# Performance work log

Measured on AMD Instinct MI355X. Metric: run time of the kernel, lower is better.

Reference implementation:

```python
import jax, jax.numpy as jnp
import numpy as np

N = 100000          # nodes
E = 3200000         # edges (avg degree 32)
IN = 256            # in_channels
H = 256             # hidden_channels == out_channels (PureConv identity lin)
STR = 60            # str_input
NUM_LOCAL = 8
NUM_LAYERS = 3


def setup_inputs() -> dict:
    key = jax.random.key(0)
    ks = jax.random.split(key, 8)
    x = jax.random.normal(ks[0], (N, IN), jnp.float32)
    pos_emb = jax.random.normal(ks[1], (N, STR), jnp.float32)
    lap_pe = jax.random.normal(ks[2], (N, STR - 1), jnp.float32)
    row = jax.random.randint(ks[3], (E,), 0, N, dtype=jnp.int32)
    col = jax.random.randint(ks[4], (E,), 0, N, dtype=jnp.int32)
    # learned params
    W_pos = jax.random.normal(ks[5], (2 * STR - 1, NUM_LOCAL), jnp.float32) * 0.1
    b_pos = jnp.zeros((NUM_LOCAL,), jnp.float32)
    W_xemb = jax.random.normal(ks[6], (IN + NUM_LOCAL, H), jnp.float32) * 0.05
    b_xemb = jnp.zeros((H,), jnp.float32)
    jkparams = jax.random.normal(ks[7], (NUM_LAYERS,), jnp.float32)
    return {
        "x": x, "pos_emb": pos_emb, "lap_pe": lap_pe,
        "W_pos": W_pos, "b_pos": b_pos, "W_xemb": W_xemb, "b_xemb": b_xemb,
        "jkparams": jkparams, "row": row, "col": col,
    }


def reference(x, pos_emb, lap_pe, W_pos, b_pos, W_xemb, b_xemb, jkparams, row, col):
    # pos_embedding: Linear(2*str_input-1 -> num_local) on cat([pos_emb, lap_pe])
    pe = jnp.concatenate([pos_emb, lap_pe], axis=-1) @ W_pos + b_pos      # [N, NUM_LOCAL]
    # xemb: Linear(in_channels + num_local -> hidden) (dropouts are identity, p=0)
    h = jnp.concatenate([x, pe], axis=-1) @ W_xemb + b_xemb               # [N, H]

    # GCN-style degree norm: norm = rsqrt(1 + rowsum(A))
    deg = jax.ops.segment_sum(jnp.ones((E,), h.dtype), row, num_segments=N)
    norm = jax.lax.rsqrt(1.0 + deg)[:, None]                              # [N, 1]

    jkx = []
    for _ in range(NUM_LAYERS):
        h = norm * h
        # spmm_add: (A @ h)[i] = sum_{edges (i<-j)} h[j]
        agg = jax.ops.segment_sum(h[col], row, num_segments=N)            # [N, H]
        h = norm * (agg + h)
        jkx.append(h)

    # jk weighted sum over layers
    out = jnp.sum(jnp.stack(jkx, axis=0) * jkparams[:, None, None], axis=0)
    return out
```

## Files before the change

kernel.cpp:

```cpp
#include <hip/hip_runtime.h>

constexpr int IN   = 256;
constexpr int H    = 256;
constexpr int STR  = 60;
constexpr int NLOC = 8;
constexpr int CHC  = 128;
constexpr int KP   = 288;
constexpr int CAP  = 96;

typedef float    f32x4 __attribute__((ext_vector_type(4)));
typedef unsigned u32x2 __attribute__((ext_vector_type(2)));
typedef short    bf16x8 __attribute__((ext_vector_type(8)));

__device__ __forceinline__ float bflo(unsigned u) { return __uint_as_float(u << 16); }
__device__ __forceinline__ float bfhi(unsigned u) { return __uint_as_float(u & 0xFFFF0000u); }
__device__ __forceinline__ unsigned short f2bf(float f) {
  unsigned u = __float_as_uint(f);
  u += 0x7FFF + ((u >> 16) & 1);
  return (unsigned short)(u >> 16);
}

__global__ void k_pe(const float* __restrict__ pos_emb, const float* __restrict__ lap_pe,
                     const float* __restrict__ W, const float* __restrict__ b,
                     float* __restrict__ pe, int n) {
  int i = blockIdx.x*blockDim.x + threadIdx.x;
  if (i >= n) return;
  float acc[NLOC];
  #pragma unroll
  for (int j = 0; j < NLOC; ++j) acc[j] = b[j];
  const float* pr = pos_emb + (size_t)i*STR;
  for (int k = 0; k < STR; ++k) {
    float v = pr[k];
    #pragma unroll
    for (int j = 0; j < NLOC; ++j) acc[j] += v*W[k*NLOC + j];
  }
  const float* lr = lap_pe + (size_t)i*(STR-1);
  for (int k = 0; k < STR-1; ++k) {
    float v = lr[k];
    #pragma unroll
    for (int j = 0; j < NLOC; ++j) acc[j] += v*W[(STR+k)*NLOC + j];
  }
  float* po = pe + (size_t)i*NLOC;
  #pragma unroll
  for (int j = 0; j < NLOC; ++j) po[j] = acc[j];
}

__global__ void k_wtb(const float* __restrict__ W, unsigned short* __restrict__ Wtb) {
  int col = blockIdx.x;
  for (int k = threadIdx.x; k < KP; k += blockDim.x) {
    float v = (k < IN + NLOC) ? W[(size_t)k*H + col] : 0.f;
    Wtb[(size_t)col*KP + k] = f2bf(v);
  }
}

__global__ void k_scatter(const int* __restrict__ row, const int* __restrict__ col,
                          int* __restrict__ cnt, int* __restrict__ colbuf, int E) {
  int i = blockIdx.x*blockDim.x + threadIdx.x;
  int stride = gridDim.x*blockDim.x;
  for (; i < E; i += stride) {
    int r = row[i];
    int p = atomicAdd(&cnt[r], 1);
    if (p < CAP) colbuf[(size_t)r*CAP + p] = col[i];
  }
}

__global__ void k_norm(const int* __restrict__ cnt, float* __restrict__ norm,
                       float* __restrict__ rnorm, int n) {
  int i = blockIdx.x*blockDim.x + threadIdx.x;
  if (i >= n) return;
  int d = cnt[i]; if (d > CAP) d = CAP;
  float s = 1.0f + (float)d;
  norm[i]  = rsqrtf(s);
  rnorm[i] = sqrtf(s);
}

__global__ __launch_bounds__(256) void k_xemb(
    const float* __restrict__ x, const float* __restrict__ pe,
    const unsigned short* __restrict__ Wtb, const float* __restrict__ bvec,
    const float* __restrict__ norm, unsigned short* __restrict__ st, int n) {
  int t = threadIdx.x;
  int wv = t >> 6, l = t & 63;
  int lr = l & 15, kb = l >> 4;
  int i0 = blockIdx.x*64 + wv*16;
  int arow = i0 + lr;
  int ar = (arow < n) ? arow : n - 1;

  f32x4 acc[16];
  #pragma unroll
  for (int cb = 0; cb < 16; ++cb) acc[cb] = (f32x4){0.f,0.f,0.f,0.f};

  const unsigned short* wb = Wtb + (size_t)lr*KP + kb*8;

  #pragma unroll
  for (int ks = 0; ks < 9; ++ks) {
    int k0 = ks*32;
    float a8[8];
    if (ks < 8) {
      const float* ap = x + (size_t)ar*IN + k0 + kb*8;
      float4 v0 = *(const float4*)ap;
      float4 v1 = *(const float4*)(ap + 4);
      a8[0]=v0.x; a8[1]=v0.y; a8[2]=v0.z; a8[3]=v0.w;
      a8[4]=v1.x; a8[5]=v1.y; a8[6]=v1.z; a8[7]=v1.w;
    } else if (kb == 0) {
      const float* ap = pe + (size_t)ar*NLOC;
      float4 v0 = *(const float4*)ap;
      float4 v1 = *(const float4*)(ap + 4);
      a8[0]=v0.x; a8[1]=v0.y; a8[2]=v0.z; a8[3]=v0.w;
      a8[4]=v1.x; a8[5]=v1.y; a8[6]=v1.z; a8[7]=v1.w;
    } else {
      #pragma unroll
      for (int j = 0; j < 8; ++j) a8[j] = 0.f;
    }
    bf16x8 af;
    #pragma unroll
    for (int j = 0; j < 8; ++j) af[j] = (short)f2bf(a8[j]);
    #pragma unroll
    for (int cb = 0; cb < 16; ++cb) {
      bf16x8 bf = *(const bf16x8*)(wb + (size_t)cb*16*KP + k0);
      acc[cb] = __builtin_amdgcn_mfma_f32_16x16x32_bf16(af, bf, acc[cb], 0, 0, 0);
    }
  }

  int r0 = i0 + kb*4;
  float nrm[4];
  #pragma unroll
  for (int j = 0; j < 4; ++j) {
    int rr = r0 + j;
    nrm[j] = (rr < n) ? norm[rr] : 0.f;
  }
  size_t slabsz = (size_t)n * CHC;
  #pragma unroll
  for (int cb = 0; cb < 16; ++cb) {
    int col = cb*16 + lr;
    float bias = bvec[col];
    unsigned short* sp = st + (size_t)(col >> 7)*slabsz + (col & 127);
    #pragma unroll
    for (int j = 0; j < 4; ++j) {
      int rr = r0 + j;
      if (rr < n)
        sp[(size_t)rr*CHC] = f2bf(nrm[j]*(acc[cb][j] + bias));
    }
  }
}

__global__ __launch_bounds__(256) void k_layer(
    const unsigned short* __restrict__ st, const int* __restrict__ cnt,
    const int* __restrict__ colbuf, const float* __restrict__ norm,
    unsigned short* __restrict__ st_next, int n, int nrb) {
  int w = blockIdx.x;
  int xcd = w & 7;
  int c = xcd >> 2;
  int rb = (w >> 3)*4 + (xcd & 3);
  if (rb >= nrb) return;
  int t = threadIdx.x;
  int wave = t >> 6, lane = t & 63, half = lane >> 5, li = lane & 31;
  int r = rb*8 + wave*2 + half;
  if (r >= n) return;
  size_t slab = (size_t)c * ((size_t)n * 32);
  const uint2* gb = (const uint2*)st + slab + li;
  int deg = cnt[r]; if (deg > CAP) deg = CAP;
  int start = r*CAP, end = start + deg;
  float4 acc = make_float4(0.f,0.f,0.f,0.f);
  int j = start;
  for (; j + 4 <= end; j += 4) {
    int c0 = colbuf[j],   c1 = colbuf[j+1];
    int c2 = colbuf[j+2], c3 = colbuf[j+3];
    uint2 v0 = gb[(size_t)c0*32];
    uint2 v1 = gb[(size_t)c1*32];
    uint2 v2 = gb[(size_t)c2*32];
    uint2 v3 = gb[(size_t)c3*32];
    acc.x += (bflo(v0.x)+bflo(v1.x)) + (bflo(v2.x)+bflo(v3.x));
    acc.y += (bfhi(v0.x)+bfhi(v1.x)) + (bfhi(v2.x)+bfhi(v3.x));
    acc.z += (bflo(v0.y)+bflo(v1.y)) + (bflo(v2.y)+bflo(v3.y));
    acc.w += (bfhi(v0.y)+bfhi(v1.y)) + (bfhi(v2.y)+bfhi(v3.y));
  }
  for (; j < end; ++j) {
    int c0 = colbuf[j];
    uint2 v0 = gb[(size_t)c0*32];
    acc.x += bflo(v0.x); acc.y += bfhi(v0.x);
    acc.z += bflo(v0.y); acc.w += bfhi(v0.y);
  }
  uint2 sv = gb[(size_t)r*32];
  acc.x += bflo(sv.x); acc.y += bfhi(sv.x);
  acc.z += bflo(sv.y); acc.w += bfhi(sv.y);
  float nr = norm[r];
  float n2 = nr*nr;
  unsigned short s0 = f2bf(n2*acc.x);
  unsigned short s1 = f2bf(n2*acc.y);
  unsigned short s2 = f2bf(n2*acc.z);
  unsigned short s3 = f2bf(n2*acc.w);
  u32x2 pk;
  pk.x = (unsigned)s0 | ((unsigned)s1 << 16);
  pk.y = (unsigned)s2 | ((unsigned)s3 << 16);
  __builtin_nontemporal_store(pk, (u32x2*)st_next + slab + (size_t)r*32 + li);
}

__global__ void k_jk(const unsigned short* __restrict__ s0,
                     const unsigned short* __restrict__ s1,
                     const unsigned short* __restrict__ s2,
                     const float* __restrict__ rnorm,
                     const float* __restrict__ jkp,
                     float* __restrict__ out, int n) {
  float j0 = jkp[0], j1 = jkp[1], j2 = jkp[2];
  size_t total = (size_t)n * 64;
  size_t idx = (size_t)blockIdx.x*blockDim.x + threadIdx.x;
  size_t stride = (size_t)gridDim.x*blockDim.x;
  for (; idx < total; idx += stride) {
    int r = (int)(idx >> 6);
    int g = (int)(idx & 63);
    int slab = g >> 5, cg = g & 31;
    size_t off = (size_t)slab*((size_t)n*32) + (size_t)r*32 + cg;
    uint2 a = ((const uint2*)s0)[off];
    uint2 b = ((const uint2*)s1)[off];
    uint2 c = ((const uint2*)s2)[off];
    float rn = rnorm[r];
    f32x4 o;
    o.x = rn*(j0*bflo(a.x) + j1*bflo(b.x) + j2*bflo(c.x));
    o.y = rn*(j0*bfhi(a.x) + j1*bfhi(b.x) + j2*bfhi(c.x));
    o.z = rn*(j0*bflo(a.y) + j1*bflo(b.y) + j2*bflo(c.y));
    o.w = rn*(j0*bfhi(a.y) + j1*bfhi(b.y) + j2*bfhi(c.y));
    *(f32x4*)(out + (size_t)r*H + slab*CHC + cg*4) = o;
  }
}

extern "C" void kernel_launch(void* const* d_in, const int* in_sizes, int n_in,
                              void* d_out, int out_size, void* d_ws, size_t ws_size,
                              hipStream_t stream) {
  const float* x       = (const float*)d_in[0];
  const float* pos_emb = (const float*)d_in[1];
  const float* lap_pe  = (const float*)d_in[2];
  const float* W_pos   = (const float*)d_in[3];
  const float* b_pos   = (const float*)d_in[4];
  const float* W_xemb  = (const float*)d_in[5];
  const float* b_xemb  = (const float*)d_in[6];
  const float* jkp     = (const float*)d_in[7];
  const int*   row     = (const int*)d_in[8];
  const int*   col     = (const int*)d_in[9];
  int N = in_sizes[0] / IN;
  int E = in_sizes[8];
  float* out = (float*)d_out;

  char* p = (char*)d_ws;
  auto alloc = [&](size_t bytes) {
    char* r = p; p += (bytes + 255) & ~(size_t)255; return r;
  };
  unsigned short* bfA = (unsigned short*)alloc((size_t)N*H*2);
  unsigned short* st0 = (unsigned short*)alloc((size_t)N*H*2);
  unsigned short* st2 = (unsigned short*)alloc((size_t)N*H*2);
  int*   colbuf = (int*)  alloc((size_t)N*CAP*4);
  float* pe     = (float*)alloc((size_t)N*NLOC*4);
  int*   cnt    = (int*)  alloc((size_t)N*4);
  float* norm   = (float*)alloc((size_t)N*4);
  float* rnorm  = (float*)alloc((size_t)N*4);
  unsigned short* Wtb = (unsigned short*)alloc((size_t)H*KP*2);

  hipMemsetAsync(cnt, 0, (size_t)N*4, stream);

  k_pe<<<(N+255)/256, 256, 0, stream>>>(pos_emb, lap_pe, W_pos, b_pos, pe, N);
  k_wtb<<<H, 128, 0, stream>>>(W_xemb, Wtb);
  k_scatter<<<2048, 256, 0, stream>>>(row, col, cnt, colbuf, E);
  k_norm<<<(N+255)/256, 256, 0, stream>>>(cnt, norm, rnorm, N);

  k_xemb<<<(N+63)/64, 256, 0, stream>>>(x, pe, Wtb, b_xemb, norm, bfA, N);

  int nrb = (N + 7)/8;
  int lgrid = 8 * ((nrb + 3)/4);
  k_layer<<<lgrid, 256, 0, stream>>>(bfA, cnt, colbuf, norm, st0, N, nrb);
  k_layer<<<lgrid, 256, 0, stream>>>(st0, cnt, colbuf, norm, bfA, N, nrb);
  k_layer<<<lgrid, 256, 0, stream>>>(bfA, cnt, colbuf, norm, st2, N, nrb);

  k_jk<<<2048, 256, 0, stream>>>(st0, bfA, st2, rnorm, jkp, out, N);
}
```

Measured before the change: 1.027 ms.

## Bucket edges before CSR fill and fuse JK sum into last layer

Edge-list construction becomes a two-pass bucketed scheme. Edges are first binned by row block of 256 into per-bucket buffers, then one workgroup per bucket fills the per-row column lists using LDS atomics and computes the degree norms in the same pass. This replaces the scattered global atomics and the separate norm kernel. The jumping-knowledge weighted sum is also fused into the third layer kernel, so the last layer's bf16 output is never written and re-read. The costs are an extra bin buffer with a fixed per-bucket capacity, which could overflow on skewed degree distributions, and a branch in the layer kernel.

```diff
diff --git a/kernel.cpp b/kernel.cpp
--- a/kernel.cpp
+++ b/kernel.cpp
@@ -7,6 +7,8 @@
 constexpr int CHC  = 128;
 constexpr int KP   = 288;
 constexpr int CAP  = 96;
+constexpr int RB   = 256;
+constexpr int BCAP = 10240;
 
 typedef float    f32x4 __attribute__((ext_vector_type(4)));
 typedef unsigned u32x2 __attribute__((ext_vector_type(2)));
@@ -53,25 +55,45 @@
   }
 }
 
-__global__ void k_scatter(const int* __restrict__ row, const int* __restrict__ col,
-                          int* __restrict__ cnt, int* __restrict__ colbuf, int E) {
+__global__ void k_bin(const int* __restrict__ row, const int* __restrict__ col,
+                      int* __restrict__ bcnt, uint2* __restrict__ binbuf, int E) {
   int i = blockIdx.x*blockDim.x + threadIdx.x;
   int stride = gridDim.x*blockDim.x;
   for (; i < E; i += stride) {
-    int r = row[i];
-    int p = atomicAdd(&cnt[r], 1);
-    if (p < CAP) colbuf[(size_t)r*CAP + p] = col[i];
-  }
-}
-
-__global__ void k_norm(const int* __restrict__ cnt, float* __restrict__ norm,
-                       float* __restrict__ rnorm, int n) {
-  int i = blockIdx.x*blockDim.x + threadIdx.x;
-  if (i >= n) return;
-  int d = cnt[i]; if (d > CAP) d = CAP;
-  float s = 1.0f + (float)d;
-  norm[i]  = rsqrtf(s);
-  rnorm[i] = sqrtf(s);
+    int r = row[i], c = col[i];
+    int b = r >> 8;
+    int p = atomicAdd(&bcnt[b], 1);
+    if (p < BCAP) binbuf[(size_t)b*BCAP + p] = make_uint2((unsigned)r, (unsigned)c);
+  }
+}
+
+__global__ __launch_bounds__(256) void k_fill(
+    const int* __restrict__ bcnt, const uint2* __restrict__ binbuf,
+    int* __restrict__ colbuf, int* __restrict__ cnt,
+    float* __restrict__ norm, float* __restrict__ rnorm, int n) {
+  __shared__ int lc[RB];
+  int b = blockIdx.x;
+  int t = threadIdx.x;
+  lc[t] = 0;
+  __syncthreads();
+  int base = b*RB;
+  int bc = bcnt[b]; if (bc > BCAP) bc = BCAP;
+  const uint2* bb = binbuf + (size_t)b*BCAP;
+  for (int i = t; i < bc; i += 256) {
+    uint2 e = bb[i];
+    int r = (int)e.x;
+    int p = atomicAdd(&lc[r - base], 1);
+    if (p < CAP) colbuf[(size_t)r*CAP + p] = (int)e.y;
+  }
+  __syncthreads();
+  int r = base + t;
+  if (r < n) {
+    int d = lc[t]; if (d > CAP) d = CAP;
+    cnt[r] = d;
+    float s = 1.0f + (float)d;
+    norm[r]  = rsqrtf(s);
+    rnorm[r] = sqrtf(s);
+  }
 }
 
 __global__ __launch_bounds__(256) void k_xemb(
@@ -146,7 +168,10 @@
 __global__ __launch_bounds__(256) void k_layer(
     const unsigned short* __restrict__ st, const int* __restrict__ cnt,
     const int* __restrict__ colbuf, const float* __restrict__ norm,
-    unsigned short* __restrict__ st_next, int n, int nrb) {
+    unsigned short* __restrict__ st_next, int last,
+    const unsigned short* __restrict__ s0buf, const unsigned short* __restrict__ s1buf,
+    const float* __restrict__ rnorm, const float* __restrict__ jkp,
+    float* __restrict__ out, int n, int nrb) {
   int w = blockIdx.x;
   int xcd = w & 7;
   int c = xcd >> 2;
@@ -158,7 +183,7 @@
   if (r >= n) return;
   size_t slab = (size_t)c * ((size_t)n * 32);
   const uint2* gb = (const uint2*)st + slab + li;
-  int deg = cnt[r]; if (deg > CAP) deg = CAP;
+  int deg = cnt[r];
   int start = r*CAP, end = start + deg;
   float4 acc = make_float4(0.f,0.f,0.f,0.f);
   int j = start;
@@ -185,41 +210,27 @@
   acc.z += bflo(sv.y); acc.w += bfhi(sv.y);
   float nr = norm[r];
   float n2 = nr*nr;
-  unsigned short s0 = f2bf(n2*acc.x);
-  unsigned short s1 = f2bf(n2*acc.y);
-  unsigned short s2 = f2bf(n2*acc.z);
-  unsigned short s3 = f2bf(n2*acc.w);
-  u32x2 pk;
-  pk.x = (unsigned)s0 | ((unsigned)s1 << 16);
-  pk.y = (unsigned)s2 | ((unsigned)s3 << 16);
-  __builtin_nontemporal_store(pk, (u32x2*)st_next + slab + (size_t)r*32 + li);
-}
-
-__global__ void k_jk(const unsigned short* __restrict__ s0,
-                     const unsigned short* __restrict__ s1,
-                     const unsigned short* __restrict__ s2,
-                     const float* __restrict__ rnorm,
-                     const float* __restrict__ jkp,
-                     float* __restrict__ out, int n) {
-  float j0 = jkp[0], j1 = jkp[1], j2 = jkp[2];
-  size_t total = (size_t)n * 64;
-  size_t idx = (size_t)blockIdx.x*blockDim.x + threadIdx.x;
-  size_t stride = (size_t)gridDim.x*blockDim.x;
-  for (; idx < total; idx += stride) {
-    int r = (int)(idx >> 6);
-    int g = (int)(idx & 63);
-    int slab = g >> 5, cg = g & 31;
-    size_t off = (size_t)slab*((size_t)n*32) + (size_t)r*32 + cg;
-    uint2 a = ((const uint2*)s0)[off];
-    uint2 b = ((const uint2*)s1)[off];
-    uint2 c = ((const uint2*)s2)[off];
+  if (!last) {
+    unsigned short s0 = f2bf(n2*acc.x);
+    unsigned short s1 = f2bf(n2*acc.y);
+    unsigned short s2 = f2bf(n2*acc.z);
+    unsigned short s3 = f2bf(n2*acc.w);
+    u32x2 pk;
+    pk.x = (unsigned)s0 | ((unsigned)s1 << 16);
+    pk.y = (unsigned)s2 | ((unsigned)s3 << 16);
+    __builtin_nontemporal_store(pk, (u32x2*)st_next + slab + (size_t)r*32 + li);
+  } else {
+    size_t off = slab + (size_t)r*32 + li;
+    uint2 a = ((const uint2*)s0buf)[off];
+    uint2 b = ((const uint2*)s1buf)[off];
     float rn = rnorm[r];
+    float j0 = jkp[0], j1 = jkp[1], j2 = jkp[2];
     f32x4 o;
-    o.x = rn*(j0*bflo(a.x) + j1*bflo(b.x) + j2*bflo(c.x));
-    o.y = rn*(j0*bfhi(a.x) + j1*bfhi(b.x) + j2*bfhi(c.x));
-    o.z = rn*(j0*bflo(a.y) + j1*bflo(b.y) + j2*bflo(c.y));
-    o.w = rn*(j0*bfhi(a.y) + j1*bfhi(b.y) + j2*bfhi(c.y));
-    *(f32x4*)(out + (size_t)r*H + slab*CHC + cg*4) = o;
+    o.x = rn*(j0*bflo(a.x) + j1*bflo(b.x) + j2*(n2*acc.x));
+    o.y = rn*(j0*bfhi(a.x) + j1*bfhi(b.x) + j2*(n2*acc.y));
+    o.z = rn*(j0*bflo(a.y) + j1*bflo(b.y) + j2*(n2*acc.z));
+    o.w = rn*(j0*bfhi(a.y) + j1*bfhi(b.y) + j2*(n2*acc.w));
+    __builtin_nontemporal_store(o, (f32x4*)(out + (size_t)r*H + c*CHC + li*4));
   }
 }
 
@@ -239,6 +250,7 @@
   int N = in_sizes[0] / IN;
   int E = in_sizes[8];
   float* out = (float*)d_out;
+  int nbuck = (N + RB - 1)/RB;
 
   char* p = (char*)d_ws;
   auto alloc = [&](size_t bytes) {
@@ -246,28 +258,30 @@
   };
   unsigned short* bfA = (unsigned short*)alloc((size_t)N*H*2);
   unsigned short* st0 = (unsigned short*)alloc((size_t)N*H*2);
-  unsigned short* st2 = (unsigned short*)alloc((size_t)N*H*2);
   int*   colbuf = (int*)  alloc((size_t)N*CAP*4);
+  uint2* binbuf = (uint2*)alloc((size_t)nbuck*BCAP*8);
   float* pe     = (float*)alloc((size_t)N*NLOC*4);
   int*   cnt    = (int*)  alloc((size_t)N*4);
+  int*   bcnt   = (int*)  alloc((size_t)nbuck*4);
   float* norm   = (float*)alloc((size_t)N*4);
   float* rnorm  = (float*)alloc((size_t)N*4);
   unsigned short* Wtb = (unsigned short*)alloc((size_t)H*KP*2);
 
-  hipMemsetAsync(cnt, 0, (size_t)N*4, stream);
-
+  hipMemsetAsync(bcnt, 0, (size_t)nbuck*4, stream);
+
+  k_bin<<<2048, 256, 0, stream>>>(row, col, bcnt, binbuf, E);
   k_pe<<<(N+255)/256, 256, 0, stream>>>(pos_emb, lap_pe, W_pos, b_pos, pe, N);
   k_wtb<<<H, 128, 0, stream>>>(W_xemb, Wtb);
-  k_scatter<<<2048, 256, 0, stream>>>(row, col, cnt, colbuf, E);
-  k_norm<<<(N+255)/256, 256, 0, stream>>>(cnt, norm, rnorm, N);
+  k_fill<<<nbuck, 256, 0, stream>>>(bcnt, binbuf, colbuf, cnt, norm, rnorm, N);
 
   k_xemb<<<(N+63)/64, 256, 0, stream>>>(x, pe, Wtb, b_xemb, norm, bfA, N);
 
   int nrb = (N + 7)/8;
   int lgrid = 8 * ((nrb + 3)/4);
-  k_layer<<<lgrid, 256, 0, stream>>>(bfA, cnt, colbuf, norm, st0, N, nrb);
-  k_layer<<<lgrid, 256, 0, stream>>>(st0, cnt, colbuf, norm, bfA, N, nrb);
-  k_layer<<<lgrid, 256, 0, stream>>>(bfA, cnt, colbuf, norm, st2, N, nrb);
-
-  k_jk<<<2048, 256, 0, stream>>>(st0, bfA, st2, rnorm, jkp, out, N);
-}
+  k_layer<<<lgrid, 256, 0, stream>>>(bfA, cnt, colbuf, norm, st0, 0,
+                                     nullptr, nullptr, nullptr, nullptr, nullptr, N, nrb);
+  k_layer<<<lgrid, 256, 0, stream>>>(st0, cnt, colbuf, norm, bfA, 0,
+                                     nullptr, nullptr, nullptr, nullptr, nullptr, N, nrb);
+  k_layer<<<lgrid, 256, 0, stream>>>(bfA, cnt, colbuf, norm, nullptr, 1,
+                                     st0, bfA, rnorm, jkp, out, N, nrb);
+}
```

After: 1.969 ms. +91.7%, slower.

## Fuse JK weighted sum into last layer and partition scatter atomics by XCD

Applied to the files above, without the earlier changes.

The final GCN layer now computes the jumping-knowledge weighted sum directly from its fp32 accumulator and the two earlier layer buffers, writing fp32 output. This removes the separate k_jk kernel along with the bf16 store and reload of the third layer. The edge scatter is also restructured so each XCD group of blocks handles only rows in its own range, which keeps atomics and colbuf writes local to one XCD. The cost is that every XCD group reads the full row array (8x the row reads), and the third layer's result is no longer rounded to bf16, which changes numerics slightly.

```diff
diff --git a/kernel.cpp b/kernel.cpp
--- a/kernel.cpp
+++ b/kernel.cpp
@@ -54,13 +54,20 @@
 }
 
 __global__ void k_scatter(const int* __restrict__ row, const int* __restrict__ col,
-                          int* __restrict__ cnt, int* __restrict__ colbuf, int E) {
-  int i = blockIdx.x*blockDim.x + threadIdx.x;
-  int stride = gridDim.x*blockDim.x;
-  for (; i < E; i += stride) {
+                          int* __restrict__ cnt, int* __restrict__ colbuf,
+                          int E, int rpx) {
+  int xcd = blockIdx.x & 7;
+  int rlo = xcd * rpx;
+  int rhi = rlo + rpx;
+  int nblk = gridDim.x >> 3;
+  int bi = blockIdx.x >> 3;
+  int stride = nblk * blockDim.x;
+  for (int i = bi*blockDim.x + threadIdx.x; i < E; i += stride) {
     int r = row[i];
-    int p = atomicAdd(&cnt[r], 1);
-    if (p < CAP) colbuf[(size_t)r*CAP + p] = col[i];
+    if (r >= rlo && r < rhi) {
+      int p = atomicAdd(&cnt[r], 1);
+      if (p < CAP) colbuf[(size_t)r*CAP + p] = col[i];
+    }
   }
 }
 
@@ -146,7 +153,10 @@
 __global__ __launch_bounds__(256) void k_layer(
     const unsigned short* __restrict__ st, const int* __restrict__ cnt,
     const int* __restrict__ colbuf, const float* __restrict__ norm,
-    unsigned short* __restrict__ st_next, int n, int nrb) {
+    unsigned short* __restrict__ st_next, int last,
+    const unsigned short* __restrict__ s0buf, const unsigned short* __restrict__ s1buf,
+    const float* __restrict__ rnorm, const float* __restrict__ jkp,
+    float* __restrict__ out, int n, int nrb) {
   int w = blockIdx.x;
   int xcd = w & 7;
   int c = xcd >> 2;
@@ -185,41 +195,27 @@
   acc.z += bflo(sv.y); acc.w += bfhi(sv.y);
   float nr = norm[r];
   float n2 = nr*nr;
-  unsigned short s0 = f2bf(n2*acc.x);
-  unsigned short s1 = f2bf(n2*acc.y);
-  unsigned short s2 = f2bf(n2*acc.z);
-  unsigned short s3 = f2bf(n2*acc.w);
-  u32x2 pk;
-  pk.x = (unsigned)s0 | ((unsigned)s1 << 16);
-  pk.y = (unsigned)s2 | ((unsigned)s3 << 16);
-  __builtin_nontemporal_store(pk, (u32x2*)st_next + slab + (size_t)r*32 + li);
-}
-
-__global__ void k_jk(const unsigned short* __restrict__ s0,
-                     const unsigned short* __restrict__ s1,
-                     const unsigned short* __restrict__ s2,
-                     const float* __restrict__ rnorm,
-                     const float* __restrict__ jkp,
-                     float* __restrict__ out, int n) {
-  float j0 = jkp[0], j1 = jkp[1], j2 = jkp[2];
-  size_t total = (size_t)n * 64;
-  size_t idx = (size_t)blockIdx.x*blockDim.x + threadIdx.x;
-  size_t stride = (size_t)gridDim.x*blockDim.x;
-  for (; idx < total; idx += stride) {
-    int r = (int)(idx >> 6);
-    int g = (int)(idx & 63);
-    int slab = g >> 5, cg = g & 31;
-    size_t off = (size_t)slab*((size_t)n*32) + (size_t)r*32 + cg;
-    uint2 a = ((const uint2*)s0)[off];
-    uint2 b = ((const uint2*)s1)[off];
-    uint2 c = ((const uint2*)s2)[off];
+  if (!last) {
+    unsigned short s0 = f2bf(n2*acc.x);
+    unsigned short s1 = f2bf(n2*acc.y);
+    unsigned short s2 = f2bf(n2*acc.z);
+    unsigned short s3 = f2bf(n2*acc.w);
+    u32x2 pk;
+    pk.x = (unsigned)s0 | ((unsigned)s1 << 16);
+    pk.y = (unsigned)s2 | ((unsigned)s3 << 16);
+    __builtin_nontemporal_store(pk, (u32x2*)st_next + slab + (size_t)r*32 + li);
+  } else {
+    size_t off = slab + (size_t)r*32 + li;
+    uint2 a = ((const uint2*)s0buf)[off];
+    uint2 b = ((const uint2*)s1buf)[off];
     float rn = rnorm[r];
+    float j0 = jkp[0], j1 = jkp[1], j2 = jkp[2];
     f32x4 o;
-    o.x = rn*(j0*bflo(a.x) + j1*bflo(b.x) + j2*bflo(c.x));
-    o.y = rn*(j0*bfhi(a.x) + j1*bfhi(b.x) + j2*bfhi(c.x));
-    o.z = rn*(j0*bflo(a.y) + j1*bflo(b.y) + j2*bflo(c.y));
-    o.w = rn*(j0*bfhi(a.y) + j1*bfhi(b.y) + j2*bfhi(c.y));
-    *(f32x4*)(out + (size_t)r*H + slab*CHC + cg*4) = o;
+    o.x = rn*(j0*bflo(a.x) + j1*bflo(b.x) + j2*(n2*acc.x));
+    o.y = rn*(j0*bfhi(a.x) + j1*bfhi(b.x) + j2*(n2*acc.y));
+    o.z = rn*(j0*bflo(a.y) + j1*bflo(b.y) + j2*(n2*acc.z));
+    o.w = rn*(j0*bfhi(a.y) + j1*bfhi(b.y) + j2*(n2*acc.w));
+    __builtin_nontemporal_store(o, (f32x4*)(out + (size_t)r*H + c*CHC + li*4));
   }
 }
 
@@ -246,7 +242,6 @@
   };
   unsigned short* bfA = (unsigned short*)alloc((size_t)N*H*2);
   unsigned short* st0 = (unsigned short*)alloc((size_t)N*H*2);
-  unsigned short* st2 = (unsigned short*)alloc((size_t)N*H*2);
   int*   colbuf = (int*)  alloc((size_t)N*CAP*4);
   float* pe     = (float*)alloc((size_t)N*NLOC*4);
   int*   cnt    = (int*)  alloc((size_t)N*4);
@@ -258,16 +253,18 @@
 
   k_pe<<<(N+255)/256, 256, 0, stream>>>(pos_emb, lap_pe, W_pos, b_pos, pe, N);
   k_wtb<<<H, 128, 0, stream>>>(W_xemb, Wtb);
-  k_scatter<<<2048, 256, 0, stream>>>(row, col, cnt, colbuf, E);
+  int rpx = (N + 7)/8;
+  k_scatter<<<1024, 256, 0, stream>>>(row, col, cnt, colbuf, E, rpx);
   k_norm<<<(N+255)/256, 256, 0, stream>>>(cnt, norm, rnorm, N);
 
   k_xemb<<<(N+63)/64, 256, 0, stream>>>(x, pe, Wtb, b_xemb, norm, bfA, N);
 
   int nrb = (N + 7)/8;
   int lgrid = 8 * ((nrb + 3)/4);
-  k_layer<<<lgrid, 256, 0, stream>>>(bfA, cnt, colbuf, norm, st0, N, nrb);
-  k_layer<<<lgrid, 256, 0, stream>>>(st0, cnt, colbuf, norm, bfA, N, nrb);
-  k_layer<<<lgrid, 256, 0, stream>>>(bfA, cnt, colbuf, norm, st2, N, nrb);
-
-  k_jk<<<2048, 256, 0, stream>>>(st0, bfA, st2, rnorm, jkp, out, N);
-}
+  k_layer<<<lgrid, 256, 0, stream>>>(bfA, cnt, colbuf, norm, st0, 0,
+                                     nullptr, nullptr, nullptr, nullptr, nullptr, N, nrb);
+  k_layer<<<lgrid, 256, 0, stream>>>(st0, cnt, colbuf, norm, bfA, 0,
+                                     nullptr, nullptr, nullptr, nullptr, nullptr, N, nrb);
+  k_layer<<<lgrid, 256, 0, stream>>>(bfA, cnt, colbuf, norm, nullptr, 1,
+                                     st0, bfA, rnorm, jkp, out, N, nrb);
+}
```

New measurement: 1.022 ms. About the same (-0.5%).
